# Kernel optimization log

Measured on AMD Instinct MI355X. Metric: run time of the kernel, lower is better.

## Reference

```python
import math
import jax, jax.numpy as jnp
import numpy as np

B, T, C, H = 1, 2048, 1024, 16
D = C // H
ROPE_THETA = 10000.0


def rope_sin_cos(t, d, theta, dtype=jnp.float32):
    # (T, D/2) sin/cos tables, standard RoPE frequencies
    inv_freq = 1.0 / (theta ** (jnp.arange(0, d, 2, dtype=jnp.float32) / d))
    ang = jnp.arange(t, dtype=jnp.float32)[:, None] * inv_freq[None, :]  # (T, D/2)
    return jnp.sin(ang).astype(dtype), jnp.cos(ang).astype(dtype)


def apply_rope(x, sin, cos):
    # x: (B, H, T, D); rotate interleaved even/odd pairs
    x1 = x[..., 0::2]
    x2 = x[..., 1::2]
    s = sin[None, None, :, :]
    c = cos[None, None, :, :]
    r1 = x1 * c - x2 * s
    r2 = x1 * s + x2 * c
    # interleave back to (..., D)
    return jnp.stack([r1, r2], axis=-1).reshape(x.shape)


def setup_inputs() -> dict:
    key = jax.random.key(0)
    k1, k2, k3 = jax.random.split(key, 3)
    x = jax.random.normal(k1, (B, T, C), dtype=jnp.float32)
    w_qkv = jax.random.normal(k2, (C, 3 * C), dtype=jnp.float32) * (1.0 / math.sqrt(C))
    w_proj = jax.random.normal(k3, (C, C), dtype=jnp.float32) * (1.0 / math.sqrt(C))
    return {"x": x, "w_qkv": w_qkv, "w_proj": w_proj}


def reference(x, w_qkv, w_proj):
    b, t, c = x.shape
    qkv = x @ w_qkv                               # (B, T, 3C)
    qkv = qkv.reshape(b, t, 3, H, D)
    q = qkv[:, :, 0].transpose(0, 2, 1, 3)        # (B, H, T, D)
    k = qkv[:, :, 1].transpose(0, 2, 1, 3)
    v = qkv[:, :, 2].transpose(0, 2, 1, 3)

    sin, cos = rope_sin_cos(t, D, ROPE_THETA, dtype=x.dtype)
    q = apply_rope(q, sin, cos)
    k = apply_rope(k, sin, cos)

    scores = jnp.einsum('bhqd,bhkd->bhqk', q, k) * (1.0 / math.sqrt(D))
    causal = jnp.tril(jnp.ones((t, t), dtype=bool))
    scores = jnp.where(causal[None, None, :, :], scores, jnp.finfo(scores.dtype).min)
    probs = jax.nn.softmax(scores, axis=-1)       # (B, H, T, T)
    out = jnp.einsum('bhqk,bhkd->bhqd', probs, v)
    out = out.transpose(0, 2, 1, 3).reshape(b, t, c)
    return out @ w_proj
```

## Files before the change

### kernel.cpp

```cpp
#include <hip/hip_runtime.h>
#include <math.h>

#define TT 2048
#define CC 1024
#define HH 16
#define DD 64
#define N3 3072

typedef unsigned short u16;
typedef __bf16 bf16x8 __attribute__((ext_vector_type(8)));
typedef float f32x4 __attribute__((ext_vector_type(4)));
typedef unsigned short u16x8 __attribute__((ext_vector_type(8)));
typedef const __attribute__((address_space(1))) void gv_t;
typedef __attribute__((address_space(3))) void lv_t;

__device__ __forceinline__ u16 bf16_rne(float f) {
  unsigned u = __float_as_uint(f);
  u += 0x7FFFu + ((u >> 16) & 1u);
  return (u16)(u >> 16);
}
__device__ __forceinline__ float bf16f(u16 h) {
  return __uint_as_float(((unsigned)h) << 16);
}
__device__ __forceinline__ bf16x8 ldfrag(const u16* p) {
  return __builtin_bit_cast(bf16x8, *(const u16x8*)p);
}
#if __has_builtin(__builtin_amdgcn_cvt_pk_bf16_f32)
__device__ __forceinline__ unsigned pk_bf16(float a, float b) {
  return __builtin_bit_cast(unsigned, __builtin_amdgcn_cvt_pk_bf16_f32(a, b));
}
#else
__device__ __forceinline__ unsigned pk_bf16(float a, float b) {
  return (unsigned)bf16_rne(a) | ((unsigned)bf16_rne(b) << 16);
}
#endif

__global__ __launch_bounds__(256) void k_prep(
    const float* __restrict__ x, const float* __restrict__ w_qkv,
    const float* __restrict__ w_proj, u16* __restrict__ xb,
    u16* __restrict__ wqkvT, u16* __restrict__ wprojT,
    float2* __restrict__ scos ) {
  __shared__ u16 tile[32][33];
  const int bi = blockIdx.x, tid = threadIdx.x;
  if (bi < 2048) {
    int i = bi * 256 + tid;
    float4 v = ((const float4*)x)[i];
    ushort4 r;
    r.x = bf16_rne(v.x); r.y = bf16_rne(v.y); r.z = bf16_rne(v.z); r.w = bf16_rne(v.w);
    ((ushort4*)xb)[i] = r;
    return;
  }
  if (bi >= 2048 + 3072 + 1024) {
    int idx = (bi - 6144) * 256 + tid;
    int t = idx >> 5, i = idx & 31;
    float inv_freq = exp2f(-(float)(2 * i) * (1.0f / 64.0f) * 13.2877123795494f);
    float ang = (float)t * inv_freq;
    scos[idx] = make_float2(sinf(ang), cosf(ang));
    return;
  }
  const int tx = tid & 31, ty = tid >> 5;
  const float* w; u16* wt; int K, N, n0, k0;
  if (bi < 2048 + 3072) {
    int b = bi - 2048; w = w_qkv; wt = wqkvT; K = CC; N = N3;
    n0 = (b % 96) * 32; k0 = (b / 96) * 32;
  } else {
    int b = bi - 5120; w = w_proj; wt = wprojT; K = CC; N = CC;
    n0 = (b & 31) * 32; k0 = (b >> 5) * 32;
  }
  for (int r = ty; r < 32; r += 8)
    tile[r][tx] = bf16_rne(w[(size_t)(k0 + r) * N + n0 + tx]);
  __syncthreads();
  for (int r = ty; r < 32; r += 8)
    wt[(size_t)(n0 + r) * K + k0 + tx] = tile[tx][r];
}

__device__ __forceinline__ bf16x8 rdsw(const u16* base, int rr, int c8) {
  return ldfrag(&base[rr * 64 + ((c8 ^ (rr & 7)) << 3)]);
}

__global__ __launch_bounds__(256) void k_gemm_qkv(
    const u16* __restrict__ A, const u16* __restrict__ Bt,
    const float2* __restrict__ scos , u16* __restrict__ qr,
    u16* __restrict__ kr, u16* __restrict__ vt, int M, int N, int K) {
  __shared__ u16 As[128 * 64];
  __shared__ u16 Bs[96 * 64];
  const int tid = threadIdx.x;
  const int lane = tid & 63, w = tid >> 6;
  const int col = lane & 15, quad = lane >> 4;
  const int wm = w >> 1, wn = w & 1;
  const int tm = blockIdx.y * 128, tn = blockIdx.x * 96;

  const int lr = lane >> 3;
  const int soff = ((lane & 7) ^ lr) << 3;

  f32x4 acc[12];
#pragma unroll
  for (int i = 0; i < 12; i++) acc[i] = (f32x4){0.f, 0.f, 0.f, 0.f};

  for (int k0 = 0; k0 < K; k0 += 64) {
#pragma unroll
    for (int i = 0; i < 4; i++) {
      const int rbase = w * 32 + i * 8;
      __builtin_amdgcn_global_load_lds(
          (gv_t*)(A + (size_t)(tm + rbase + lr) * K + k0 + soff),
          (lv_t*)(&As[rbase * 64]), 16, 0, 0);
    }
#pragma unroll
    for (int i = 0; i < 3; i++) {
      const int rbase = w * 24 + i * 8;
      __builtin_amdgcn_global_load_lds(
          (gv_t*)(Bt + (size_t)(tn + rbase + lr) * K + k0 + soff),
          (lv_t*)(&Bs[rbase * 64]), 16, 0, 0);
    }
    __syncthreads();
#pragma unroll
    for (int kk = 0; kk < 2; kk++) {
      bf16x8 af[4], bf[3];
#pragma unroll
      for (int mt = 0; mt < 4; mt++)
        af[mt] = rdsw(As, wm * 64 + mt * 16 + col, kk * 4 + quad);
#pragma unroll
      for (int nt = 0; nt < 3; nt++)
        bf[nt] = rdsw(Bs, wn * 48 + nt * 16 + col, kk * 4 + quad);
#pragma unroll
      for (int mt = 0; mt < 4; mt++)
#pragma unroll
        for (int nt = 0; nt < 3; nt++)
          acc[mt * 3 + nt] = __builtin_amdgcn_mfma_f32_16x16x32_bf16(af[mt], bf[nt], acc[mt * 3 + nt], 0, 0, 0);
    }
    __syncthreads();
  }

  const int tb = tm + wm * 64;
#pragma unroll
  for (int nt = 0; nt < 3; nt++) {
    const int nn = tn + wn * 48 + nt * 16;
    const int slice = nn >> 10;
    const int hh = (nn >> 6) & 15;
    const int db = nn & 63;
    const int d = db + col;
    if (slice < 2) {
      u16* dst = (slice == 0) ? qr : kr;
      const bool ev = (col & 1) == 0;
      const int i = (db >> 1) + (col >> 1);
#pragma unroll
      for (int mt = 0; mt < 4; mt++)
#pragma unroll
        for (int r = 0; r < 4; r++) {
          int t = tb + mt * 16 + quad * 4 + r;
          float2 sc2 = scos[t * 32 + i];
          float e = acc[mt * 3 + nt][r];
          float pp = __shfl_xor(e, 1);
          float v = ev ? (e * sc2.y - pp * sc2.x) : (pp * sc2.x + e * sc2.y);
          dst[((size_t)(hh * TT + t) << 6) + d] = bf16_rne(v);
        }
    } else {
#pragma unroll
      for (int mt = 0; mt < 4; mt++)
#pragma unroll
        for (int r = 0; r < 4; r++) {
          int t = tb + mt * 16 + quad * 4 + r;
          vt[((size_t)(hh * DD + d)) * TT + t] = bf16_rne(acc[mt * 3 + nt][r]);
        }
    }
  }
}

__global__ __launch_bounds__(256) void k_gemm_pj(
    const u16* __restrict__ A, const u16* __restrict__ Bt,
    float* __restrict__ C, int M, int N, int K) {
  __shared__ u16 As[128 * 64];
  __shared__ u16 Bs[64 * 64];
  const int tid = threadIdx.x;
  const int lane = tid & 63, w = tid >> 6;
  const int col = lane & 15, quad = lane >> 4;
  const int tm = blockIdx.y * 128, tn = blockIdx.x * 64;

  const int lr = lane >> 3;
  const int soff = ((lane & 7) ^ lr) << 3;

  f32x4 acc[8];
#pragma unroll
  for (int i = 0; i < 8; i++) acc[i] = (f32x4){0.f, 0.f, 0.f, 0.f};

  for (int k0 = 0; k0 < K; k0 += 64) {
#pragma unroll
    for (int i = 0; i < 4; i++) {
      const int rbase = w * 32 + i * 8;
      __builtin_amdgcn_global_load_lds(
          (gv_t*)(A + (size_t)(tm + rbase + lr) * K + k0 + soff),
          (lv_t*)(&As[rbase * 64]), 16, 0, 0);
    }
#pragma unroll
    for (int i = 0; i < 2; i++) {
      const int rbase = w * 16 + i * 8;
      __builtin_amdgcn_global_load_lds(
          (gv_t*)(Bt + (size_t)(tn + rbase + lr) * K + k0 + soff),
          (lv_t*)(&Bs[rbase * 64]), 16, 0, 0);
    }
    __syncthreads();
#pragma unroll
    for (int kk = 0; kk < 2; kk++) {
      bf16x8 af[2], bf[4];
#pragma unroll
      for (int mt = 0; mt < 2; mt++)
        af[mt] = rdsw(As, w * 32 + mt * 16 + col, kk * 4 + quad);
#pragma unroll
      for (int nt = 0; nt < 4; nt++)
        bf[nt] = rdsw(Bs, nt * 16 + col, kk * 4 + quad);
#pragma unroll
      for (int mt = 0; mt < 2; mt++)
#pragma unroll
        for (int nt = 0; nt < 4; nt++)
          acc[mt * 4 + nt] = __builtin_amdgcn_mfma_f32_16x16x32_bf16(af[mt], bf[nt], acc[mt * 4 + nt], 0, 0, 0);
    }
    __syncthreads();
  }
#pragma unroll
  for (int mt = 0; mt < 2; mt++)
#pragma unroll
    for (int nt = 0; nt < 4; nt++)
#pragma unroll
      for (int r = 0; r < 4; r++)
        C[(size_t)(tm + w * 32 + mt * 16 + quad * 4 + r) * N + tn + nt * 16 + col] =
            acc[mt * 4 + nt][r];
}

__global__ __launch_bounds__(256) void k_flash(
    const u16* __restrict__ qr, const u16* __restrict__ kr,
    const u16* __restrict__ vt, u16* __restrict__ attnb ) {
  __shared__ u16 Ks[2][2][64 * 64];
  __shared__ u16 Vs[2][2][64 * 64];
  __shared__ u16 Ps[4][16 * 64];

  const int tid = threadIdx.x;
  const int lane = tid & 63, wv = tid >> 6;
  const int col = lane & 15, quad = lane >> 4;

  const int bid = blockIdx.x;
  const int xcd = bid & 7, slot = bid >> 3;
  const int cu = slot & 31, half = slot >> 5;
  const int rank = half ? (63 - cu) : cu;
  const int sp = 31 - (rank >> 1);
  const int h = xcd * 2 + (rank & 1);
  const int q0 = sp * 64;
  const int nkt = sp + 1;
  const int nw = (nkt + 1) >> 1;

  const u16* Qh = qr + (size_t)h * TT * DD;
  const u16* Kh = kr + (size_t)h * TT * DD;
  const u16* Vh = vt + (size_t)h * DD * TT;

  const bf16x8 aq0 = ldfrag(&Qh[(size_t)(q0 + wv * 16 + col) * DD + quad * 8]);
  const bf16x8 aq1 = ldfrag(&Qh[(size_t)(q0 + wv * 16 + col) * DD + 32 + quad * 8]);

  const int lr = lane >> 3;
  const int srcoff = ((lane & 7) ^ lr) << 3;

  auto stage = [&](int win, int buf) {
    const int k0 = win * 128;
#pragma unroll
    for (int j = 0; j < 2; j++) {
#pragma unroll
      for (int i = 0; i < 2; i++) {
        const int rbase = wv * 16 + i * 8;
        __builtin_amdgcn_global_load_lds(
            (gv_t*)(Kh + (size_t)(k0 + j * 64 + rbase + lr) * DD + srcoff),
            (lv_t*)(&Ks[buf][j][rbase * 64]), 16, 0, 0);
        __builtin_amdgcn_global_load_lds(
            (gv_t*)(Vh + (size_t)(rbase + lr) * TT + k0 + j * 64 + srcoff),
            (lv_t*)(&Vs[buf][j][rbase * 64]), 16, 0, 0);
      }
    }
  };

  const f32x4 zero = {0.f, 0.f, 0.f, 0.f};
  f32x4 acc[4] = {zero, zero, zero, zero};
  float lpart[4] = {0.f, 0.f, 0.f, 0.f};
  u16* Pb = &Ps[wv][0];

  auto compute = [&](int k0j, const u16* Kt, const u16* Vt) {
    f32x4 sc[4];
#pragma unroll
    for (int nt = 0; nt < 4; nt++) {
      const int rr = nt * 16 + col;
      sc[nt] = __builtin_amdgcn_mfma_f32_16x16x32_bf16(aq0, rdsw(Kt, rr, quad), zero, 0, 0, 0);
      sc[nt] = __builtin_amdgcn_mfma_f32_16x16x32_bf16(aq1, rdsw(Kt, rr, 4 + quad), sc[nt], 0, 0, 0);
    }
    if (k0j == q0) {
#pragma unroll
      for (int nt = 0; nt < 4; nt++)
#pragma unroll
        for (int r = 0; r < 4; r++)
          if (nt * 16 + col > wv * 16 + quad * 4 + r) sc[nt][r] = -1e30f;
    }
#pragma unroll
    for (int nt = 0; nt < 4; nt++)
#pragma unroll
      for (int r = 0; r < 4; r++) {
        float p = exp2f(fmaf(sc[nt][r], 0.18033688f, -28.8539008f));
        sc[nt][r] = p;
        lpart[r] += p;
      }
#pragma unroll
    for (int nt = 0; nt < 4; nt++) {
      unsigned p01 = pk_bf16(sc[nt][0], sc[nt][1]);
      unsigned p23 = pk_bf16(sc[nt][2], sc[nt][3]);
      u16* base = Pb + quad * 4 * 64 + ((nt ^ quad) << 4) + col;
      base[0 * 64] = (u16)p01;
      base[1 * 64] = (u16)(p01 >> 16);
      base[2 * 64] = (u16)p23;
      base[3 * 64] = (u16)(p23 >> 16);
    }
#pragma unroll
    for (int kk = 0; kk < 2; kk++) {
      int sb = (kk * 2 + (quad >> 1)) ^ (col >> 2);
      bf16x8 ap = ldfrag(&Pb[col * 64 + (sb << 4) + ((quad & 1) << 3)]);
#pragma unroll
      for (int nt = 0; nt < 4; nt++)
        acc[nt] = __builtin_amdgcn_mfma_f32_16x16x32_bf16(
            ap, rdsw(Vt, nt * 16 + col, kk * 4 + quad), acc[nt], 0, 0, 0);
    }
  };

  stage(0, 0);
  for (int win = 0; win < nw; win++) {
    const int buf = win & 1;
    __syncthreads();
    if (win + 1 < nw) stage(win + 1, buf ^ 1);
#pragma unroll
    for (int j = 0; j < 2; j++) {
      const int k0j = win * 128 + j * 64;
      if (k0j <= q0) compute(k0j, Ks[buf][j], Vs[buf][j]);
    }
  }

#pragma unroll
  for (int o = 1; o < 16; o <<= 1)
#pragma unroll
    for (int r = 0; r < 4; r++) lpart[r] += __shfl_xor(lpart[r], o);
  float inv[4];
#pragma unroll
  for (int r = 0; r < 4; r++) inv[r] = 1.f / lpart[r];
#pragma unroll
  for (int nt = 0; nt < 4; nt++)
#pragma unroll
    for (int r = 0; r < 4; r++) {
      int q = q0 + wv * 16 + quad * 4 + r;
      attnb[(size_t)q * CC + h * DD + nt * 16 + col] = bf16_rne(acc[nt][r] * inv[r]);
    }
}

extern "C" void kernel_launch(void* const* d_in, const int* in_sizes, int n_in,
                              void* d_out, int out_size, void* d_ws, size_t ws_size,
                              hipStream_t stream) {
  const float* x      = (const float*)d_in[0];
  const float* w_qkv  = (const float*)d_in[1];
  const float* w_proj = (const float*)d_in[2];
  float* out = (float*)d_out;

  char* p = (char*)d_ws;
  u16* xb      = (u16*)p;    p += (size_t)TT * CC * 2;
  u16* wqkvT   = (u16*)p;    p += (size_t)N3 * CC * 2;
  u16* wprojT  = (u16*)p;    p += (size_t)CC * CC * 2;
  float2* scos = (float2*)p; p += (size_t)TT * 32 * 8;
  u16* qr      = (u16*)p;    p += (size_t)HH * TT * DD * 2;
  u16* kr      = (u16*)p;    p += (size_t)HH * TT * DD * 2;
  u16* vt      = (u16*)p;    p += (size_t)HH * DD * TT * 2;
  u16* attnb   = (u16*)p;    p += (size_t)TT * CC * 2;

  k_prep<<<2048 + 3072 + 1024 + 256, 256, 0, stream>>>(x, w_qkv, w_proj, xb, wqkvT, wprojT, scos);
  k_gemm_qkv<<<dim3(N3 / 96, TT / 128), 256, 0, stream>>>(xb, wqkvT, scos, qr, kr, vt, TT, N3, CC);
  k_flash<<<512, 256, 0, stream>>>(qr, kr, vt, attnb);
  k_gemm_pj<<<dim3(CC / 64, TT / 128), 256, 0, stream>>>(attnb, wprojT, out, TT, CC, CC);
}
```

Baseline: 149.6 us.

## Double-buffer GEMM shared-memory tiles and widen weight-transpose stores in prep

Both bf16 GEMM kernels now use two LDS buffers per operand. The next K-tile's global-to-LDS load is issued before the MFMAs on the current tile, so load latency can overlap with compute. This doubles LDS per block, which may lower occupancy. The prep kernel's weight transpose now handles 64x32 tiles and writes 4-element vector stores, halving the number of transpose blocks and cutting narrow scattered writes.

```diff
diff --git a/kernel.cpp b/kernel.cpp
--- a/kernel.cpp
+++ b/kernel.cpp
@@ -40,7 +40,7 @@
     const float* __restrict__ w_proj, u16* __restrict__ xb,
     u16* __restrict__ wqkvT, u16* __restrict__ wprojT,
     float2* __restrict__ scos ) {
-  __shared__ u16 tile[32][33];
+  __shared__ u16 tile[64][34];
   const int bi = blockIdx.x, tid = threadIdx.x;
   if (bi < 2048) {
     int i = bi * 256 + tid;
@@ -50,28 +50,40 @@
     ((ushort4*)xb)[i] = r;
     return;
   }
-  if (bi >= 2048 + 3072 + 1024) {
-    int idx = (bi - 6144) * 256 + tid;
+  if (bi >= 2048 + 1536 + 512) {
+    int idx = (bi - 4096) * 256 + tid;
     int t = idx >> 5, i = idx & 31;
     float inv_freq = exp2f(-(float)(2 * i) * (1.0f / 64.0f) * 13.2877123795494f);
     float ang = (float)t * inv_freq;
     scos[idx] = make_float2(sinf(ang), cosf(ang));
     return;
   }
-  const int tx = tid & 31, ty = tid >> 5;
   const float* w; u16* wt; int K, N, n0, k0;
-  if (bi < 2048 + 3072) {
+  if (bi < 2048 + 1536) {
     int b = bi - 2048; w = w_qkv; wt = wqkvT; K = CC; N = N3;
-    n0 = (b % 96) * 32; k0 = (b / 96) * 32;
+    k0 = (b / 96) * 64; n0 = (b % 96) * 32;
   } else {
-    int b = bi - 5120; w = w_proj; wt = wprojT; K = CC; N = CC;
-    n0 = (b & 31) * 32; k0 = (b >> 5) * 32;
-  }
-  for (int r = ty; r < 32; r += 8)
-    tile[r][tx] = bf16_rne(w[(size_t)(k0 + r) * N + n0 + tx]);
+    int b = bi - 3584; w = w_proj; wt = wprojT; K = CC; N = CC;
+    k0 = (b >> 5) * 64; n0 = (b & 31) * 32;
+  }
+  const int tx = tid & 31, r0 = tid >> 5;
+#pragma unroll
+  for (int j = 0; j < 8; j++) {
+    int k = r0 + j * 8;
+    tile[k][tx] = bf16_rne(w[(size_t)(k0 + k) * N + n0 + tx]);
+  }
   __syncthreads();
-  for (int r = ty; r < 32; r += 8)
-    wt[(size_t)(n0 + r) * K + k0 + tx] = tile[tx][r];
+  const int kc = tid & 15, nr = tid >> 4;
+#pragma unroll
+  for (int jn = 0; jn < 2; jn++) {
+    int n = nr + (jn << 4);
+    ushort4 o;
+    o.x = tile[kc * 4 + 0][n];
+    o.y = tile[kc * 4 + 1][n];
+    o.z = tile[kc * 4 + 2][n];
+    o.w = tile[kc * 4 + 3][n];
+    *(ushort4*)&wt[(size_t)(n0 + n) * K + k0 + kc * 4] = o;
+  }
 }
 
 __device__ __forceinline__ bf16x8 rdsw(const u16* base, int rr, int c8) {
@@ -82,8 +94,8 @@
     const u16* __restrict__ A, const u16* __restrict__ Bt,
     const float2* __restrict__ scos , u16* __restrict__ qr,
     u16* __restrict__ kr, u16* __restrict__ vt, int M, int N, int K) {
-  __shared__ u16 As[128 * 64];
-  __shared__ u16 Bs[96 * 64];
+  __shared__ u16 As[2][128 * 64];
+  __shared__ u16 Bs[2][96 * 64];
   const int tid = threadIdx.x;
   const int lane = tid & 63, w = tid >> 6;
   const int col = lane & 15, quad = lane >> 4;
@@ -97,31 +109,38 @@
 #pragma unroll
   for (int i = 0; i < 12; i++) acc[i] = (f32x4){0.f, 0.f, 0.f, 0.f};
 
-  for (int k0 = 0; k0 < K; k0 += 64) {
+  auto stage = [&](int k0, int buf) {
 #pragma unroll
     for (int i = 0; i < 4; i++) {
       const int rbase = w * 32 + i * 8;
       __builtin_amdgcn_global_load_lds(
           (gv_t*)(A + (size_t)(tm + rbase + lr) * K + k0 + soff),
-          (lv_t*)(&As[rbase * 64]), 16, 0, 0);
+          (lv_t*)(&As[buf][rbase * 64]), 16, 0, 0);
     }
 #pragma unroll
     for (int i = 0; i < 3; i++) {
       const int rbase = w * 24 + i * 8;
       __builtin_amdgcn_global_load_lds(
           (gv_t*)(Bt + (size_t)(tn + rbase + lr) * K + k0 + soff),
-          (lv_t*)(&Bs[rbase * 64]), 16, 0, 0);
-    }
-    __syncthreads();
+          (lv_t*)(&Bs[buf][rbase * 64]), 16, 0, 0);
+    }
+  };
+
+  stage(0, 0);
+  __syncthreads();
+  const int NT = K / 64;
+  for (int t = 0; t < NT; t++) {
+    const int cur = t & 1;
+    if (t + 1 < NT) stage((t + 1) * 64, cur ^ 1);
 #pragma unroll
     for (int kk = 0; kk < 2; kk++) {
       bf16x8 af[4], bf[3];
 #pragma unroll
       for (int mt = 0; mt < 4; mt++)
-        af[mt] = rdsw(As, wm * 64 + mt * 16 + col, kk * 4 + quad);
+        af[mt] = rdsw(&As[cur][0], wm * 64 + mt * 16 + col, kk * 4 + quad);
 #pragma unroll
       for (int nt = 0; nt < 3; nt++)
-        bf[nt] = rdsw(Bs, wn * 48 + nt * 16 + col, kk * 4 + quad);
+        bf[nt] = rdsw(&Bs[cur][0], wn * 48 + nt * 16 + col, kk * 4 + quad);
 #pragma unroll
       for (int mt = 0; mt < 4; mt++)
 #pragma unroll
@@ -169,8 +188,8 @@
 __global__ __launch_bounds__(256) void k_gemm_pj(
     const u16* __restrict__ A, const u16* __restrict__ Bt,
     float* __restrict__ C, int M, int N, int K) {
-  __shared__ u16 As[128 * 64];
-  __shared__ u16 Bs[64 * 64];
+  __shared__ u16 As[2][128 * 64];
+  __shared__ u16 Bs[2][64 * 64];
   const int tid = threadIdx.x;
   const int lane = tid & 63, w = tid >> 6;
   const int col = lane & 15, quad = lane >> 4;
@@ -183,31 +202,38 @@
 #pragma unroll
   for (int i = 0; i < 8; i++) acc[i] = (f32x4){0.f, 0.f, 0.f, 0.f};
 
-  for (int k0 = 0; k0 < K; k0 += 64) {
+  auto stage = [&](int k0, int buf) {
 #pragma unroll
     for (int i = 0; i < 4; i++) {
       const int rbase = w * 32 + i * 8;
       __builtin_amdgcn_global_load_lds(
           (gv_t*)(A + (size_t)(tm + rbase + lr) * K + k0 + soff),
-          (lv_t*)(&As[rbase * 64]), 16, 0, 0);
+          (lv_t*)(&As[buf][rbase * 64]), 16, 0, 0);
     }
 #pragma unroll
     for (int i = 0; i < 2; i++) {
       const int rbase = w * 16 + i * 8;
       __builtin_amdgcn_global_load_lds(
           (gv_t*)(Bt + (size_t)(tn + rbase + lr) * K + k0 + soff),
-          (lv_t*)(&Bs[rbase * 64]), 16, 0, 0);
-    }
-    __syncthreads();
+          (lv_t*)(&Bs[buf][rbase * 64]), 16, 0, 0);
+    }
+  };
+
+  stage(0, 0);
+  __syncthreads();
+  const int NT = K / 64;
+  for (int t = 0; t < NT; t++) {
+    const int cur = t & 1;
+    if (t + 1 < NT) stage((t + 1) * 64, cur ^ 1);
 #pragma unroll
     for (int kk = 0; kk < 2; kk++) {
       bf16x8 af[2], bf[4];
 #pragma unroll
       for (int mt = 0; mt < 2; mt++)
-        af[mt] = rdsw(As, w * 32 + mt * 16 + col, kk * 4 + quad);
+        af[mt] = rdsw(&As[cur][0], w * 32 + mt * 16 + col, kk * 4 + quad);
 #pragma unroll
       for (int nt = 0; nt < 4; nt++)
-        bf[nt] = rdsw(Bs, nt * 16 + col, kk * 4 + quad);
+        bf[nt] = rdsw(&Bs[cur][0], nt * 16 + col, kk * 4 + quad);
 #pragma unroll
       for (int mt = 0; mt < 2; mt++)
 #pragma unroll
@@ -369,7 +395,7 @@
   u16* vt      = (u16*)p;    p += (size_t)HH * DD * TT * 2;
   u16* attnb   = (u16*)p;    p += (size_t)TT * CC * 2;
 
-  k_prep<<<2048 + 3072 + 1024 + 256, 256, 0, stream>>>(x, w_qkv, w_proj, xb, wqkvT, wprojT, scos);
+  k_prep<<<2048 + 1536 + 512 + 256, 256, 0, stream>>>(x, w_qkv, w_proj, xb, wqkvT, wprojT, scos);
   k_gemm_qkv<<<dim3(N3 / 96, TT / 128), 256, 0, stream>>>(xb, wqkvT, scos, qr, kr, vt, TT, N3, CC);
   k_flash<<<512, 256, 0, stream>>>(qr, kr, vt, attnb);
   k_gemm_pj<<<dim3(CC / 64, TT / 128), 256, 0, stream>>>(attnb, wprojT, out, TT, CC, CC);
```

Measured after the change: 144.4 us. 3.5% less time.
